# Performance work log

Hardware: AMD Instinct MI355X
Metric: run time of the kernel (lower is better)

The kernel has to match this reference:

```python
import jax, jax.numpy as jnp
import numpy as np

D_IN = 4096
D_OUT = 4096
R = 8  # Tucker core rank per mode
M = 16  # tensor mode size (16^3 = 4096)


def setup_inputs() -> dict:
    key = jax.random.key(0)
    ks = jax.random.split(key, 12)
    inp = {}
    inp['x'] = jax.random.normal(ks[0], (4, 2048, D_IN), dtype=jnp.float32)
    inp['core'] = jax.random.normal(ks[1], (R,) * 6, dtype=jnp.float32) * 0.1
    for i, name in enumerate(['fo0', 'fo1', 'fo2', 'fi0', 'fi1', 'fi2']):
        inp[name] = jax.random.normal(ks[2 + i], (M, R), dtype=jnp.float32) * (1.0 / np.sqrt(M))
    inp['bias'] = jax.random.normal(ks[8], (D_OUT,), dtype=jnp.float32) * 0.01
    inp['alpha'] = jnp.ones((1,), dtype=jnp.float32)
    inp['per_dim_scale'] = jnp.ones((D_OUT,), dtype=jnp.float32)
    input_perm = jax.random.permutation(ks[9], D_IN).astype(jnp.int32)
    output_perm = jax.random.permutation(ks[10], D_OUT)
    inp['input_perm'] = input_perm
    inp['output_inv_perm'] = jnp.argsort(output_perm).astype(jnp.int32)
    return inp


def _tucker_to_matrix(core, fo0, fo1, fo2, fi0, fi1, fi2):
    # W_tensor = core x1 fo0 x2 fo1 x3 fo2 x4 fi0 x5 fi1 x6 fi2
    W = jnp.einsum('abcdef,Aa,Bb,Cc,Dd,Ee,Ff->ABCDEF',
                   core, fo0, fo1, fo2, fi0, fi1, fi2)
    return W.reshape(D_OUT, D_IN)


def reference(x, core, fo0, fo1, fo2, fi0, fi1, fi2,
              bias, alpha, per_dim_scale, input_perm, output_inv_perm):
    W = _tucker_to_matrix(core, fo0, fo1, fo2, fi0, fi1, fi2)  # permuted-space weight
    lead = x.shape[:-1]
    xf = x.reshape(-1, D_IN)[:, input_perm]          # apply input channel permutation
    out = xf @ W.T                                   # [tokens, D_OUT] in permuted space
    out = out[:, output_inv_perm]                    # back to original channel order
    out = out * alpha * per_dim_scale + bias
    return out.reshape(lead + (D_OUT,))
```

## Files before the change

kernel.cpp:

```cpp
#include <hip/hip_runtime.h>
#include <hip/hip_bf16.h>


#define DIN 4096
#define DOUT 4096

typedef __bf16 bf16x8 __attribute__((ext_vector_type(8)));
typedef float f32x4 __attribute__((ext_vector_type(4)));

static __device__ __forceinline__ unsigned int f2bf(float f) {
    unsigned int u = __builtin_bit_cast(unsigned int, f);
    u += 0x7fffu + ((u >> 16) & 1u);
    return u >> 16;
}

static __device__ __forceinline__ void gld16(const void* g, void* l) {
    __builtin_amdgcn_global_load_lds(
        (const __attribute__((address_space(1))) void*)g,
        (__attribute__((address_space(3))) void*)l, 16, 0, 0);
}

__global__ __launch_bounds__(256) void tucker_kP(
    const float* __restrict__ G,
    const float* __restrict__ fo0,
    const float* __restrict__ fo1,
    const float* __restrict__ fo2,
    const float* __restrict__ pds,
    const float* __restrict__ alpha,
    const int*   __restrict__ oinv,
    unsigned short* __restrict__ Bm)
{
    __shared__ float Gk[512 * 4];
    __shared__ float W1[1024 * 4];
    __shared__ float W2[2048 * 4];
    __shared__ float W3[4096 * 4];
    __shared__ float fos[3 * 128];
    const int t = threadIdx.x;
    const int k0 = blockIdx.x * 4;

    if (t < 128) {
        fos[t]       = fo0[t];
        fos[128 + t] = fo1[t];
        fos[256 + t] = fo2[t];
    }
#pragma unroll
    for (int i = 0; i < 2; ++i) {
        const int g = t + 256 * i;
        *(float4*)(Gk + g * 4) = *(const float4*)(G + (size_t)g * 512 + k0);
    }
    __syncthreads();

#pragma unroll
    for (int i = 0; i < 4; ++i) {
        const int o = t + 256 * i;
        const int A = o >> 6, bc = o & 63;
        float4 acc = make_float4(0.f, 0.f, 0.f, 0.f);
#pragma unroll
        for (int a = 0; a < 8; ++a) {
            const float f = fos[A * 8 + a];
            const float4 g4 = *(const float4*)(Gk + (a * 64 + bc) * 4);
            acc.x += f * g4.x; acc.y += f * g4.y; acc.z += f * g4.z; acc.w += f * g4.w;
        }
        *(float4*)(W1 + o * 4) = acc;
    }
    __syncthreads();

#pragma unroll
    for (int i = 0; i < 8; ++i) {
        const int o = t + 256 * i;
        const int A = o >> 7, B = (o >> 3) & 15, c = o & 7;
        float4 acc = make_float4(0.f, 0.f, 0.f, 0.f);
#pragma unroll
        for (int b = 0; b < 8; ++b) {
            const float f = fos[128 + B * 8 + b];
            const float4 g4 = *(const float4*)(W1 + (A * 64 + b * 8 + c) * 4);
            acc.x += f * g4.x; acc.y += f * g4.y; acc.z += f * g4.z; acc.w += f * g4.w;
        }
        *(float4*)(W2 + o * 4) = acc;
    }
    __syncthreads();

#pragma unroll
    for (int i = 0; i < 16; ++i) {
        const int o = t + 256 * i;
        const int A = o >> 8, B = (o >> 4) & 15, C = o & 15;
        float4 acc = make_float4(0.f, 0.f, 0.f, 0.f);
#pragma unroll
        for (int c = 0; c < 8; ++c) {
            const float f = fos[256 + C * 8 + c];
            const float4 g4 = *(const float4*)(W2 + ((A * 16 + B) * 8 + c) * 4);
            acc.x += f * g4.x; acc.y += f * g4.y; acc.z += f * g4.z; acc.w += f * g4.w;
        }
        *(float4*)(W3 + o * 4) = acc;
    }
    __syncthreads();

    const float alf = alpha[0];
#pragma unroll
    for (int i = 0; i < 16; ++i) {
        const int j = t + 256 * i;
        const float s = alf * pds[j];
        const float4 v = *(const float4*)(W3 + (size_t)oinv[j] * 4);
        uint2 pk;
        pk.x = f2bf(v.x * s) | (f2bf(v.y * s) << 16);
        pk.y = f2bf(v.z * s) | (f2bf(v.w * s) << 16);
        *(uint2*)(Bm + (size_t)j * 512 + k0) = pk;
    }
}

__global__ __launch_bounds__(256) void tucker_kA(
    const float* __restrict__ x,
    const int*   __restrict__ iperm,
    const float* __restrict__ fi0,
    const float* __restrict__ fi1,
    const float* __restrict__ fi2,
    unsigned short* __restrict__ t3o)
{
    __shared__ float xs[4096];
    __shared__ float t1[8 * 272];
    __shared__ float t2[8 * 136];
    const int t = threadIdx.x;
    const int n = blockIdx.x;

    {
        const float4* x4 = (const float4*)(x + (size_t)n * DIN);
        float4* xs4 = (float4*)xs;
#pragma unroll
        for (int i = 0; i < 4; ++i) xs4[t + 256 * i] = x4[t + 256 * i];
    }
    __syncthreads();

    {
        float acc[8];
#pragma unroll
        for (int d = 0; d < 8; ++d) acc[d] = 0.f;
#pragma unroll 4
        for (int D = 0; D < 16; ++D) {
            const int pg = iperm[D * 256 + t];
            const float v = xs[pg];
#pragma unroll
            for (int d = 0; d < 8; ++d) acc[d] += v * fi0[D * 8 + d];
        }
#pragma unroll
        for (int d = 0; d < 8; ++d) t1[d * 272 + t] = acc[d];
    }
    __syncthreads();

    if (t < 128) {
        const int d = t >> 4, F = t & 15;
        float acc[8];
#pragma unroll
        for (int e = 0; e < 8; ++e) acc[e] = 0.f;
#pragma unroll 4
        for (int E = 0; E < 16; ++E) {
            const float v = t1[d * 272 + E * 16 + F];
#pragma unroll
            for (int e = 0; e < 8; ++e) acc[e] += v * fi1[E * 8 + e];
        }
#pragma unroll
        for (int e = 0; e < 8; ++e) t2[d * 136 + e * 17 + F] = acc[e];
    }
    __syncthreads();

    if (t < 64) {
        const int d = t >> 3, e = t & 7;
        float acc[8];
#pragma unroll
        for (int f = 0; f < 8; ++f) acc[f] = 0.f;
#pragma unroll 4
        for (int F = 0; F < 16; ++F) {
            const float v = t2[d * 136 + e * 17 + F];
#pragma unroll
            for (int f = 0; f < 8; ++f) acc[f] += v * fi2[F * 8 + f];
        }
        uint4 pk;
        pk.x = f2bf(acc[0]) | (f2bf(acc[1]) << 16);
        pk.y = f2bf(acc[2]) | (f2bf(acc[3]) << 16);
        pk.z = f2bf(acc[4]) | (f2bf(acc[5]) << 16);
        pk.w = f2bf(acc[6]) | (f2bf(acc[7]) << 16);
        *(uint4*)(t3o + (size_t)n * 512 + t * 8) = pk;
    }
}

__global__ __launch_bounds__(256) void tucker_kG(
    const unsigned short* __restrict__ A,
    const unsigned short* __restrict__ B,
    const float* __restrict__ bias,
    float* __restrict__ out,
    int gm)
{
    __shared__ __align__(16) unsigned short As[128 * 64];
    __shared__ __align__(16) unsigned short Bs[128 * 64];
    const int t = threadIdx.x;
    const int mt = blockIdx.x % gm;
    const int nt = blockIdx.x / gm;
    const size_t r0 = (size_t)mt * 128;
    const size_t n0 = (size_t)nt * 128;
    const int lane = t & 63, w = t >> 6;
    const int wr = (w >> 1) * 64, wc = (w & 1) * 64;
    const int ml = lane & 15, kq = lane >> 4;

    const unsigned short* Ab = A + r0 * 512;
    const unsigned short* Bb = B + n0 * 512;

    f32x4 acc[4][4];
#pragma unroll
    for (int m = 0; m < 4; ++m)
#pragma unroll
        for (int n = 0; n < 4; ++n) acc[m][n] = (f32x4){0.f, 0.f, 0.f, 0.f};

    for (int kt = 0; kt < 8; ++kt) {
        const int kc0 = kt * 64;
#pragma unroll
        for (int i = 0; i < 4; ++i) {
            const int cc = t + 256 * i;
            const int row = cc >> 3;
            const int sg = (cc & 7) ^ (row & 7);
            gld16(Ab + (size_t)row * 512 + kc0 + sg * 8, As + cc * 8);
            gld16(Bb + (size_t)row * 512 + kc0 + sg * 8, Bs + cc * 8);
        }
        __syncthreads();

#pragma unroll
        for (int ks = 0; ks < 2; ++ks) {
            bf16x8 af[4], bv[4];
#pragma unroll
            for (int m = 0; m < 4; ++m) {
                const int row = wr + m * 16 + ml;
                af[m] = *(const bf16x8*)(As + row * 64 + ((((ks << 2) + kq)) ^ (row & 7)) * 8);
            }
#pragma unroll
            for (int n = 0; n < 4; ++n) {
                const int row = wc + n * 16 + ml;
                bv[n] = *(const bf16x8*)(Bs + row * 64 + ((((ks << 2) + kq)) ^ (row & 7)) * 8);
            }
#pragma unroll
            for (int m = 0; m < 4; ++m)
#pragma unroll
                for (int n = 0; n < 4; ++n)
                    acc[m][n] = __builtin_amdgcn_mfma_f32_16x16x32_bf16(af[m], bv[n], acc[m][n], 0, 0, 0);
        }
        __syncthreads();
    }

#pragma unroll
    for (int n = 0; n < 4; ++n) {
        const size_t col = n0 + wc + n * 16 + ml;
        const float bval = bias[col];
#pragma unroll
        for (int m = 0; m < 4; ++m) {
            const size_t rowb = r0 + wr + m * 16 + kq * 4;
#pragma unroll
            for (int r = 0; r < 4; ++r)
                out[(rowb + r) * DOUT + col] = acc[m][n][r] + bval;
        }
    }
}

extern "C" void kernel_launch(void* const* d_in, const int* in_sizes, int n_in,
                              void* d_out, int out_size, void* d_ws, size_t ws_size,
                              hipStream_t stream) {
    const float* x    = (const float*)d_in[0];
    const float* core = (const float*)d_in[1];
    const float* fo0  = (const float*)d_in[2];
    const float* fo1  = (const float*)d_in[3];
    const float* fo2  = (const float*)d_in[4];
    const float* fi0  = (const float*)d_in[5];
    const float* fi1  = (const float*)d_in[6];
    const float* fi2  = (const float*)d_in[7];
    const float* bias = (const float*)d_in[8];
    const float* alpha= (const float*)d_in[9];
    const float* pds  = (const float*)d_in[10];
    const int* iperm  = (const int*)d_in[11];
    const int* oinv   = (const int*)d_in[12];
    float* out = (float*)d_out;

    const int nrows = in_sizes[0] / DIN;

    unsigned short* Bm = (unsigned short*)d_ws;
    unsigned short* t3 = (unsigned short*)d_ws + (2u << 20);

    tucker_kP<<<128, 256, 0, stream>>>(core, fo0, fo1, fo2, pds, alpha, oinv, Bm);
    tucker_kA<<<nrows, 256, 0, stream>>>(x, iperm, fi0, fi1, fi2, t3);
    const int gm = nrows / 128;
    tucker_kG<<<gm * (DOUT / 128), 256, 0, stream>>>(t3, Bm, bias, out, gm);
}
```

Baseline: 339.7 us.

## Triple-buffer GEMM tiles with async LDS loads and widen block to 128x256

The bf16 GEMM kernel now uses 512 threads on a 128x256 output tile and keeps three LDS stages, so global-to-LDS loads run two k-steps ahead of the MFMA work. Explicit vmcnt waits and raw barriers replace the two __syncthreads per iteration, and setprio raises wave priority around the MFMA block. This targets load latency and barrier stalls in the K=512 GEMM, in exchange for much more LDS (about 144KB) and fewer resident blocks. The hand-counted vmcnt value must match the number of outstanding loads per thread.

```diff
diff --git a/kernel.cpp b/kernel.cpp
--- a/kernel.cpp
+++ b/kernel.cpp
@@ -182,66 +182,93 @@
     }
 }
 
-__global__ __launch_bounds__(256) void tucker_kG(
+__global__ __launch_bounds__(512) void tucker_kG(
     const unsigned short* __restrict__ A,
     const unsigned short* __restrict__ B,
     const float* __restrict__ bias,
     float* __restrict__ out,
     int gm)
 {
-    __shared__ __align__(16) unsigned short As[128 * 64];
-    __shared__ __align__(16) unsigned short Bs[128 * 64];
+    __shared__ __align__(16) unsigned short As[3][128 * 64];
+    __shared__ __align__(16) unsigned short Bs[3][256 * 64];
     const int t = threadIdx.x;
     const int mt = blockIdx.x % gm;
     const int nt = blockIdx.x / gm;
     const size_t r0 = (size_t)mt * 128;
-    const size_t n0 = (size_t)nt * 128;
+    const size_t n0 = (size_t)nt * 256;
     const int lane = t & 63, w = t >> 6;
-    const int wr = (w >> 1) * 64, wc = (w & 1) * 64;
+    const int wr = (w >> 2) * 64;
+    const int wc = (w & 3) * 64;
     const int ml = lane & 15, kq = lane >> 4;
 
     const unsigned short* Ab = A + r0 * 512;
     const unsigned short* Bb = B + n0 * 512;
 
+#define STAGE_TILE(b, kt)  do {                                              \
+        const int kc_ = (kt) * 64;                                           \
+        _Pragma("unroll")                                                    \
+        for (int i_ = 0; i_ < 2; ++i_) {                                     \
+            const int c_ = t + 512 * i_;                                     \
+            const int row_ = c_ >> 3, sl_ = c_ & 7;                          \
+            const int sg_ = sl_ ^ (row_ & 7);                                \
+            gld16(Ab + (size_t)row_ * 512 + kc_ + sg_ * 8, As[b] + c_ * 8);  \
+        }                                                                    \
+        _Pragma("unroll")                                                    \
+        for (int i_ = 0; i_ < 4; ++i_) {                                     \
+            const int c_ = t + 512 * i_;                                     \
+            const int row_ = c_ >> 3, sl_ = c_ & 7;                          \
+            const int sg_ = sl_ ^ (row_ & 7);                                \
+            gld16(Bb + (size_t)row_ * 512 + kc_ + sg_ * 8, Bs[b] + c_ * 8);  \
+        }                                                                    \
+    } while (0)
+
     f32x4 acc[4][4];
 #pragma unroll
     for (int m = 0; m < 4; ++m)
 #pragma unroll
         for (int n = 0; n < 4; ++n) acc[m][n] = (f32x4){0.f, 0.f, 0.f, 0.f};
 
+    STAGE_TILE(0, 0);
+    STAGE_TILE(1, 1);
+
     for (int kt = 0; kt < 8; ++kt) {
-        const int kc0 = kt * 64;
-#pragma unroll
-        for (int i = 0; i < 4; ++i) {
-            const int cc = t + 256 * i;
-            const int row = cc >> 3;
-            const int sg = (cc & 7) ^ (row & 7);
-            gld16(Ab + (size_t)row * 512 + kc0 + sg * 8, As + cc * 8);
-            gld16(Bb + (size_t)row * 512 + kc0 + sg * 8, Bs + cc * 8);
-        }
-        __syncthreads();
-
+        __builtin_amdgcn_sched_barrier(0);
+        if (kt < 7) asm volatile("s_waitcnt vmcnt(6) lgkmcnt(0)" ::: "memory");
+        else        asm volatile("s_waitcnt vmcnt(0) lgkmcnt(0)" ::: "memory");
+        __builtin_amdgcn_s_barrier();
+        __builtin_amdgcn_sched_barrier(0);
+
+        if (kt < 6) {
+            const int nb = (kt + 2) % 3;
+            STAGE_TILE(nb, kt + 2);
+        }
+        __builtin_amdgcn_sched_barrier(0);
+
+        const unsigned short* Ax = As[kt % 3];
+        const unsigned short* Bx = Bs[kt % 3];
 #pragma unroll
         for (int ks = 0; ks < 2; ++ks) {
             bf16x8 af[4], bv[4];
 #pragma unroll
             for (int m = 0; m < 4; ++m) {
                 const int row = wr + m * 16 + ml;
-                af[m] = *(const bf16x8*)(As + row * 64 + ((((ks << 2) + kq)) ^ (row & 7)) * 8);
+                af[m] = *(const bf16x8*)(Ax + row * 64 + ((((ks << 2) + kq)) ^ (row & 7)) * 8);
             }
 #pragma unroll
             for (int n = 0; n < 4; ++n) {
                 const int row = wc + n * 16 + ml;
-                bv[n] = *(const bf16x8*)(Bs + row * 64 + ((((ks << 2) + kq)) ^ (row & 7)) * 8);
+                bv[n] = *(const bf16x8*)(Bx + row * 64 + ((((ks << 2) + kq)) ^ (row & 7)) * 8);
             }
+            __builtin_amdgcn_s_setprio(1);
 #pragma unroll
             for (int m = 0; m < 4; ++m)
 #pragma unroll
                 for (int n = 0; n < 4; ++n)
                     acc[m][n] = __builtin_amdgcn_mfma_f32_16x16x32_bf16(af[m], bv[n], acc[m][n], 0, 0, 0);
-        }
-        __syncthreads();
-    }
+            __builtin_amdgcn_s_setprio(0);
+        }
+    }
+#undef STAGE_TILE
 
 #pragma unroll
     for (int n = 0; n < 4; ++n) {
@@ -283,5 +310,5 @@
     tucker_kP<<<128, 256, 0, stream>>>(core, fo0, fo1, fo2, pds, alpha, oinv, Bm);
     tucker_kA<<<nrows, 256, 0, stream>>>(x, iperm, fi0, fi1, fi2, t3);
     const int gm = nrows / 128;
-    tucker_kG<<<gm * (DOUT / 128), 256, 0, stream>>>(t3, Bm, bias, out, gm);
-}
+    tucker_kG<<<gm * (DOUT / 256), 512, 0, stream>>>(t3, Bm, bias, out, gm);
+}
```

Result: no change. 342.6 us (+0.8%).
